# Kernel tuning notes

Hardware: AMD Instinct MI355X
Metric: run time of the kernel (lower is better)

The kernel has to match this reference:

```python
import jax, jax.numpy as jnp
import numpy as np

N, E, G = 10000, 160000, 64      # nodes, edges, graphs
IN, H, L = 128, 128, 14          # in_channels, hidden, num GENConv layers
EPS_LN = 1e-5                    # torch LayerNorm eps
EPS_MSG = 1e-7                   # GENConv message eps


def layer_norm(x, g, b):
    mu = jnp.mean(x, axis=-1, keepdims=True)
    v = jnp.var(x, axis=-1, keepdims=True)
    return (x - mu) * jax.lax.rsqrt(v + EPS_LN) * g + b


def gen_conv(h, src, dst, t, sc, W1, b1, mg, mb, W2, b2):
    # message: relu(x_j) + eps  (no edge_attr)
    msg = jax.nn.relu(h[src]) + EPS_MSG                      # [E, H]
    # softmax aggregation over edges sharing a destination, per feature
    z = msg * t
    mx = jax.ops.segment_max(z, dst, num_segments=N)         # [N, H]
    mx = jnp.where(jnp.isfinite(mx), mx, 0.0)
    e = jnp.exp(z - mx[dst])
    ssum = jax.ops.segment_sum(e, dst, num_segments=N)
    alpha = e / (ssum[dst] + 1e-16)
    agg = jax.ops.segment_sum(msg * alpha, dst, num_segments=N)  # [N, H]
    # MessageNorm: normalize(agg) * ||h|| * scale
    agg = agg / jnp.maximum(jnp.linalg.norm(agg, axis=-1, keepdims=True), 1e-12)
    agg = agg * jnp.linalg.norm(h, axis=-1, keepdims=True) * sc
    out = h + agg
    # MLP [H, 2H, H] with LayerNorm + ReLU between (dropout off in eval)
    z1 = layer_norm(out @ W1 + b1, mg, mb)
    return jax.nn.relu(z1) @ W2 + b2


def setup_inputs() -> dict:
    key = jax.random.key(0)
    ks = jax.random.split(key, 8)
    s = 0.05
    x = jax.random.normal(ks[0], (N, IN), jnp.float32)
    edge_index = jax.random.randint(ks[1], (2, E), 0, N, dtype=jnp.int64)
    batch = jnp.sort(jax.random.randint(ks[2], (N,), 0, G, dtype=jnp.int64))
    enc_W = jax.random.normal(ks[3], (IN, H), jnp.float32) * s
    enc_b = jnp.zeros((H,), jnp.float32)
    ln_g = jnp.ones((L, H), jnp.float32)
    ln_b = jnp.zeros((L, H), jnp.float32)
    t = jnp.ones((L,), jnp.float32)         # learnable softmax temperature
    scale = jnp.ones((L,), jnp.float32)     # learnable MsgNorm scale
    W1 = jax.random.normal(ks[4], (L, H, 2 * H), jnp.float32) * s
    b1 = jnp.zeros((L, 2 * H), jnp.float32)
    mg = jnp.ones((L, 2 * H), jnp.float32)
    mb = jnp.zeros((L, 2 * H), jnp.float32)
    W2 = jax.random.normal(ks[5], (L, 2 * H, H), jnp.float32) * s
    b2 = jnp.zeros((L, H), jnp.float32)
    fn_g = jnp.ones((H,), jnp.float32)
    fn_b = jnp.zeros((H,), jnp.float32)
    return dict(x=x, edge_index=edge_index, batch=batch, enc_W=enc_W, enc_b=enc_b,
                ln_g=ln_g, ln_b=ln_b, t=t, scale=scale, W1=W1, b1=b1, mg=mg, mb=mb,
                W2=W2, b2=b2, fn_g=fn_g, fn_b=fn_b)


def reference(x, edge_index, batch, enc_W, enc_b, ln_g, ln_b, t, scale,
              W1, b1, mg, mb, W2, b2, fn_g, fn_b):
    src, dst = edge_index[0], edge_index[1]
    h = x @ enc_W + enc_b
    for i in range(L):  # DeepGCNLayer 'res+': x + conv(act(norm(x)))
        r = jax.nn.leaky_relu(layer_norm(h, ln_g[i], ln_b[i]), 0.01)
        h = h + gen_conv(r, src, dst, t[i], scale[i],
                         W1[i], b1[i], mg[i], mb[i], W2[i], b2[i])
    h = jax.nn.leaky_relu(layer_norm(h, fn_g, fn_b), 0.01)
    # global_mean_pool (fin_map is unused in the original forward)
    cnt = jax.ops.segment_sum(jnp.ones((N,), h.dtype), batch, num_segments=G)
    gf = jax.ops.segment_sum(h, batch, num_segments=G) / jnp.maximum(cnt, 1.0)[:, None]
    return gf
```

## Files before the change

### kernel.cpp

```cpp
#include <hip/hip_runtime.h>
#include <cstdint>
#include <cstddef>


#define BT 512

typedef __attribute__((ext_vector_type(8))) short bf16x8;
typedef __attribute__((ext_vector_type(4))) float f32x4;

__device__ inline float bf2f(ushort u) {
    union { uint i; float f; } v;
    v.i = (uint)u << 16;
    return v.f;
}
__device__ inline ushort f2bf(float f) {
    union { float f; uint i; } v;
    v.f = f;
    return (ushort)((v.i + 0x7fffu + ((v.i >> 16) & 1u)) >> 16);
}
__device__ inline uint f2bf2(float a, float b) {
    return (uint)f2bf(a) | ((uint)f2bf(b) << 16);
}
__device__ inline float fast_exp2(float x) {
    return __builtin_amdgcn_exp2f(x);
}

__device__ inline float wave_sum_f(float v) {
#pragma unroll
    for (int off = 32; off > 0; off >>= 1) v += __shfl_xor(v, off, 64);
    return v;
}

__global__ void setup_kernel(const float* __restrict__ x, ushort* __restrict__ xb,
                             const int* __restrict__ dst, int* __restrict__ deg,
                             const int* __restrict__ batch, int* __restrict__ gstart,
                             int total, int N, int E, int G) {
    int idx = blockIdx.x * blockDim.x + threadIdx.x;
    if (idx >= total) return;
    xb[idx] = f2bf(x[idx]);
    if (idx < E) atomicAdd(&deg[dst[idx]], 1);
    if (idx < N) {
        int bb = batch[idx];
        if (idx == 0)
            for (int g = 0; g <= bb; g++) gstart[g] = 0;
        else {
            int pb = batch[idx - 1];
            for (int g = pb + 1; g <= bb; g++) gstart[g] = idx;
        }
        if (idx == N - 1)
            for (int g = bb + 1; g <= G; g++) gstart[g] = N;
    }
}

__global__ __launch_bounds__(1024) void scan_kernel(const int* __restrict__ deg,
                                                    int* __restrict__ offs,
                                                    int* __restrict__ cursor, int N) {
    __shared__ int part[1024];
    int tid = threadIdx.x;
    int CH = (N + 1023) / 1024;
    int base = tid * CH;
    int s = 0;
    for (int i = 0; i < CH; i++) {
        int idx = base + i;
        if (idx < N) s += deg[idx];
    }
    part[tid] = s;
    __syncthreads();
    for (int off = 1; off < 1024; off <<= 1) {
        int v = (tid >= off) ? part[tid - off] : 0;
        __syncthreads();
        part[tid] += v;
        __syncthreads();
    }
    int run = (tid == 0) ? 0 : part[tid - 1];
    for (int i = 0; i < CH; i++) {
        int idx = base + i;
        if (idx < N) {
            offs[idx] = run;
            cursor[idx] = run;
            run += deg[idx];
        }
    }
    if (tid == 1023) offs[N] = part[1023];
}

__global__ void scatter_kernel(const int* __restrict__ src, const int* __restrict__ dst,
                               int* __restrict__ cursor, int* __restrict__ esrc, int E) {
    int e = blockIdx.x * blockDim.x + threadIdx.x;
    if (e < E) {
        int d = dst[e];
        int pos = atomicAdd(&cursor[d], 1);
        esrc[pos] = src[e];
    }
}

__global__ __launch_bounds__(256) void prep_kernel(const float* __restrict__ W1,
                                                   const float* __restrict__ W2,
                                                   const float* __restrict__ encW,
                                                   ushort* __restrict__ W1t,
                                                   ushort* __restrict__ W2t,
                                                   ushort* __restrict__ encWt, int L) {
    __shared__ float tile[32][33];
    int z = blockIdx.z;
    const float* in;
    ushort* out;
    int R, C;
    if (z < L) {
        in = W1 + (size_t)z * 32768; out = W1t + (size_t)z * 32768; R = 128; C = 256;
    } else if (z < 2 * L) {
        int i = z - L;
        in = W2 + (size_t)i * 32768; out = W2t + (size_t)i * 32768; R = 256; C = 128;
    } else {
        in = encW; out = encWt; R = 128; C = 128;
    }
    int r0 = blockIdx.y * 32, c0 = blockIdx.x * 32;
    if (r0 >= R || c0 >= C) return;
    int tx = threadIdx.x & 31, ty = threadIdx.x >> 5;
    for (int i = ty; i < 32; i += 8) tile[i][tx] = in[(size_t)(r0 + i) * C + c0 + tx];
    __syncthreads();
    for (int i = ty; i < 32; i += 8)
        out[(size_t)(c0 + i) * R + r0 + tx] = f2bf(tile[tx][i]);
}

__device__ __forceinline__ void agg_stage_v18(const ushort* __restrict__ rin,
                                              const int* __restrict__ offs,
                                              const int* __restrict__ esrc,
                                              const float* __restrict__ rnbuf,
                                              float tv2, float sv,
                                              int row0, int w, int l,
                                              uint (*AsU)[68]) {
    const uint2* rin2 = (const uint2*)rin;
    int nd0 = row0 + 2 * w;
    int half = l >> 5, li = l & 31;
    int a0 = offs[nd0], a1 = offs[nd0 + 1], a2 = offs[nd0 + 2];
    int eb[2] = {a0, a1};
    int dg[2] = {a1 - a0, a2 - a1};

    uint2 ru0 = rin2[(size_t)nd0 * 32 + li];
    uint2 ru1 = rin2[(size_t)(nd0 + 1) * 32 + li];
    float rn0 = rnbuf[nd0], rn1 = rnbuf[nd0 + 1];

    float s[2][4] = {}, W[2][4] = {};
    int mxdeg = max(dg[0], dg[1]);

#pragma unroll 1
    for (int base = 0; base < mxdeg; base += 64) {
        int rem0 = min(dg[0] - base, 64);
        int rem1 = min(dg[1] - base, 64);
        int idx0 = (rem0 > 0 && l < rem0) ? esrc[eb[0] + base + l] : 0;
        int idx1 = (rem1 > 0 && l < rem1) ? esrc[eb[1] + base + l] : 0;
        int it = (max(rem0, rem1) + 7) >> 3;
#pragma unroll 1
        for (int i = 0; i < it; i++) {
            int j0 = i * 8 + half;
            uint2 rv[2][4];
            bool vl[2][4];
#pragma unroll
            for (int c = 0; c < 4; c++) {
                int j = j0 + 2 * c;
                vl[0][c] = j < rem0;
                vl[1][c] = j < rem1;
                int sn0 = __shfl(idx0, j, 64);
                int sn1 = __shfl(idx1, j, 64);
                if (vl[0][c]) rv[0][c] = rin2[(size_t)sn0 * 32 + li];
                if (vl[1][c]) rv[1][c] = rin2[(size_t)sn1 * 32 + li];
            }
#pragma unroll
            for (int k = 0; k < 2; k++)
#pragma unroll
                for (int c = 0; c < 4; c++) {
                    if (vl[k][c]) {
                        float f0 = bf2f((ushort)(rv[k][c].x & 0xffff));
                        float f1 = bf2f((ushort)(rv[k][c].x >> 16));
                        float f2 = bf2f((ushort)(rv[k][c].y & 0xffff));
                        float f3 = bf2f((ushort)(rv[k][c].y >> 16));
                        float g0 = fmaxf(f0, 0.f) + 1e-7f;
                        float g1 = fmaxf(f1, 0.f) + 1e-7f;
                        float g2 = fmaxf(f2, 0.f) + 1e-7f;
                        float g3 = fmaxf(f3, 0.f) + 1e-7f;
                        float p0 = fast_exp2(g0 * tv2);
                        float p1 = fast_exp2(g1 * tv2);
                        float p2 = fast_exp2(g2 * tv2);
                        float p3 = fast_exp2(g3 * tv2);
                        s[k][0] += p0; W[k][0] += g0 * p0;
                        s[k][1] += p1; W[k][1] += g1 * p1;
                        s[k][2] += p2; W[k][2] += g2 * p2;
                        s[k][3] += p3; W[k][3] += g3 * p3;
                    }
                }
        }
    }

#pragma unroll
    for (int k = 0; k < 2; k++) {
#pragma unroll
        for (int f = 0; f < 4; f++) {
            s[k][f] += __shfl_xor(s[k][f], 32, 64);
            W[k][f] += __shfl_xor(W[k][f], 32, 64);
        }
        float agg[4], nsq = 0.f;
#pragma unroll
        for (int f = 0; f < 4; f++) {
            agg[f] = W[k][f] / (s[k][f] + 1e-16f);
            nsq += agg[f] * agg[f];
        }
#pragma unroll
        for (int off = 1; off < 32; off <<= 1) nsq += __shfl_xor(nsq, off, 64);
        float rnv = (k == 0) ? rn0 : rn1;
        uint2 ru = (k == 0) ? ru0 : ru1;
        float fac = rnv * sv / fmaxf(sqrtf(nsq), 1e-12f);
        if (half == 0) {
            uint2 o;
            o.x = f2bf2(bf2f((ushort)(ru.x & 0xffff)) + agg[0] * fac,
                        bf2f((ushort)(ru.x >> 16)) + agg[1] * fac);
            o.y = f2bf2(bf2f((ushort)(ru.y & 0xffff)) + agg[2] * fac,
                        bf2f((ushort)(ru.y >> 16)) + agg[3] * fac);
            *(uint2*)&AsU[2 * w + k][2 * li] = o;
        }
    }
}

__device__ __forceinline__ void gemm1_stage8(const ushort (*As)[136],
                                             const ushort* __restrict__ Bt,
                                             const float* __restrict__ bias,
                                             const float* __restrict__ mg,
                                             const float* __restrict__ mb,
                                             ushort (*z1s)[264],
                                             int w, int q, int ln,
                                             float (*pS)[16], float (*pQ)[16]) {
    f32x4 acc[2];
    acc[0] = (f32x4){0.f, 0.f, 0.f, 0.f};
    acc[1] = (f32x4){0.f, 0.f, 0.f, 0.f};
#pragma unroll
    for (int ks = 0; ks < 128; ks += 32) {
        bf16x8 a = *(const bf16x8*)&As[ln][ks + q * 8];
#pragma unroll
        for (int ct = 0; ct < 2; ct++) {
            bf16x8 bv = *(const bf16x8*)(Bt + (size_t)(w * 32 + ct * 16 + ln) * 128 + ks + q * 8);
            acc[ct] = __builtin_amdgcn_mfma_f32_16x16x32_bf16(a, bv, acc[ct], 0, 0, 0);
        }
    }
    float s1[4] = {0, 0, 0, 0}, s2[4] = {0, 0, 0, 0};
#pragma unroll
    for (int ct = 0; ct < 2; ct++)
#pragma unroll
        for (int r = 0; r < 4; r++) {
            float v = acc[ct][r] + bias[w * 32 + ct * 16 + ln];
            acc[ct][r] = v;
            s1[r] += v;
            s2[r] += v * v;
        }
#pragma unroll
    for (int off = 1; off < 16; off <<= 1)
#pragma unroll
        for (int r = 0; r < 4; r++) {
            s1[r] += __shfl_xor(s1[r], off, 64);
            s2[r] += __shfl_xor(s2[r], off, 64);
        }
    if (ln == 0)
#pragma unroll
        for (int r = 0; r < 4; r++) {
            pS[w][q * 4 + r] = s1[r];
            pQ[w][q * 4 + r] = s2[r];
        }
    __syncthreads();
#pragma unroll
    for (int r = 0; r < 4; r++) {
        int row = q * 4 + r;
        float S = 0.f, Q = 0.f;
#pragma unroll
        for (int ww = 0; ww < 8; ww++) {
            S += pS[ww][row];
            Q += pQ[ww][row];
        }
        float mu = S * (1.f / 256.f);
        float var = Q * (1.f / 256.f) - mu * mu;
        float rs = rsqrtf(var + 1e-5f);
#pragma unroll
        for (int ct = 0; ct < 2; ct++) {
            int col = w * 32 + ct * 16 + ln;
            float y = (acc[ct][r] - mu) * rs * mg[col] + mb[col];
            z1s[row][col] = f2bf(fmaxf(y, 0.f));
        }
    }
    __syncthreads();
}

template <int KD, bool RESID>
__device__ __forceinline__ void out_stage8(const ushort* __restrict__ Abase, int astr,
                                           const ushort* __restrict__ Bt,
                                           const float* __restrict__ bias,
                                           const float* __restrict__ lg,
                                           const float* __restrict__ lb,
                                           float* __restrict__ hbuf,
                                           ushort* __restrict__ rout,
                                           float* __restrict__ rnbuf,
                                           int row0, int w, int q, int ln,
                                           float (*pS)[16], float (*pQ)[16]) {
    f32x4 acc = (f32x4){0.f, 0.f, 0.f, 0.f};
    int col = w * 16 + ln;
#pragma unroll
    for (int ks = 0; ks < KD; ks += 32) {
        bf16x8 a = *(const bf16x8*)(Abase + ln * astr + ks + q * 8);
        bf16x8 bv = *(const bf16x8*)(Bt + (size_t)col * KD + ks + q * 8);
        acc = __builtin_amdgcn_mfma_f32_16x16x32_bf16(a, bv, acc, 0, 0, 0);
    }
    float s1[4], s2[4];
#pragma unroll
    for (int r = 0; r < 4; r++) {
        int row = q * 4 + r;
        float v = acc[r] + bias[col];
        if (RESID) v += hbuf[(size_t)(row0 + row) * 128 + col];
        hbuf[(size_t)(row0 + row) * 128 + col] = v;
        acc[r] = v;
        s1[r] = v;
        s2[r] = v * v;
    }
#pragma unroll
    for (int off = 1; off < 16; off <<= 1)
#pragma unroll
        for (int r = 0; r < 4; r++) {
            s1[r] += __shfl_xor(s1[r], off, 64);
            s2[r] += __shfl_xor(s2[r], off, 64);
        }
    if (ln == 0)
#pragma unroll
        for (int r = 0; r < 4; r++) {
            pS[w][q * 4 + r] = s1[r];
            pQ[w][q * 4 + r] = s2[r];
        }
    __syncthreads();
    float yv[4];
    float t2[4];
#pragma unroll
    for (int r = 0; r < 4; r++) {
        int row = q * 4 + r;
        float S = 0.f, Q = 0.f;
#pragma unroll
        for (int ww = 0; ww < 8; ww++) {
            S += pS[ww][row];
            Q += pQ[ww][row];
        }
        float mu = S * (1.f / 128.f);
        float var = Q * (1.f / 128.f) - mu * mu;
        float rs = rsqrtf(var + 1e-5f);
        float y = (acc[r] - mu) * rs * lg[col] + lb[col];
        y = y > 0.f ? y : 0.01f * y;
        yv[r] = y;
        t2[r] = y * y;
    }
#pragma unroll
    for (int off = 1; off < 16; off <<= 1)
#pragma unroll
        for (int r = 0; r < 4; r++) t2[r] += __shfl_xor(t2[r], off, 64);
    __syncthreads();
    if (ln == 0)
#pragma unroll
        for (int r = 0; r < 4; r++) pS[w][q * 4 + r] = t2[r];
    __syncthreads();
#pragma unroll
    for (int r = 0; r < 4; r++) {
        int row = q * 4 + r;
        float T = 0.f;
#pragma unroll
        for (int ww = 0; ww < 8; ww++) T += pS[ww][row];
        if (w == 0 && ln == 0) rnbuf[row0 + row] = sqrtf(T);
        rout[(size_t)(row0 + row) * 128 + col] = f2bf(yv[r]);
    }
}

__global__ __launch_bounds__(BT) void enc_kernel(const ushort* __restrict__ xb,
                                                 const ushort* __restrict__ encWt,
                                                 const float* __restrict__ encB,
                                                 const float* __restrict__ lg,
                                                 const float* __restrict__ lb,
                                                 float* __restrict__ h,
                                                 ushort* __restrict__ rbuf,
                                                 float* __restrict__ rn, int N) {
    __shared__ __align__(16) ushort As[16][136];
    __shared__ float pS[8][16], pQ[8][16];
    uint(*AsU)[68] = (uint(*)[68])As;
    int tid = threadIdx.x, w = tid >> 6, l = tid & 63;
    int q = l >> 4, ln = l & 15;
    int row0 = blockIdx.x * 16;
    for (int idx = tid; idx < 16 * 64; idx += BT) {
        int row = idx >> 6, cl = idx & 63;
        AsU[row][cl] = ((const uint*)xb)[(size_t)(row0 + row) * 64 + cl];
    }
    __syncthreads();
    out_stage8<128, false>(&As[0][0], 136, encWt, encB, lg, lb, h, rbuf, rn,
                           row0, w, q, ln, pS, pQ);
}

__global__ __launch_bounds__(BT) void layer_kernel(const ushort* __restrict__ rin,
                                                   ushort* __restrict__ rout,
                                                   const int* __restrict__ offs,
                                                   const int* __restrict__ esrc,
                                                   float* __restrict__ rn,
                                                   float* __restrict__ h,
                                                   const ushort* __restrict__ W1t,
                                                   const ushort* __restrict__ W2t,
                                                   const float* __restrict__ b1,
                                                   const float* __restrict__ mg,
                                                   const float* __restrict__ mb,
                                                   const float* __restrict__ b2,
                                                   const float* __restrict__ ng,
                                                   const float* __restrict__ nb,
                                                   const float* __restrict__ tptr,
                                                   const float* __restrict__ scptr,
                                                   int N) {
    __shared__ __align__(16) ushort As[16][136];
    __shared__ __align__(16) ushort z1s[16][264];
    __shared__ float pS[8][16], pQ[8][16];
    uint(*AsU)[68] = (uint(*)[68])As;
    int tid = threadIdx.x, w = tid >> 6, l = tid & 63;
    int q = l >> 4, ln = l & 15;
    int row0 = blockIdx.x * 16;
    float tv2 = (*tptr) * 1.4426950408889634f;
    float sv = *scptr;
    agg_stage_v18(rin, offs, esrc, rn, tv2, sv, row0, w, l, AsU);
    __syncthreads();
    gemm1_stage8(As, W1t, b1, mg, mb, z1s, w, q, ln, pS, pQ);
    out_stage8<256, true>(&z1s[0][0], 264, W2t, b2, ng, nb, h, rout, rn,
                          row0, w, q, ln, pS, pQ);
}

__global__ __launch_bounds__(256) void pool_kernel(const ushort* __restrict__ rf,
                                                   const int* __restrict__ gstart,
                                                   float* __restrict__ out) {
    __shared__ float pb0[4][64], pb1[4][64];
    int g = blockIdx.x;
    int w = threadIdx.x >> 6, l = threadIdx.x & 63;
    int s = gstart[g], e = gstart[g + 1];
    float a0 = 0.f, a1 = 0.f;
    for (int n = s + w; n < e; n += 4) {
        uint rv = ((const uint*)rf)[(size_t)n * 64 + l];
        a0 += bf2f((ushort)(rv & 0xffff));
        a1 += bf2f((ushort)(rv >> 16));
    }
    pb0[w][l] = a0;
    pb1[w][l] = a1;
    __syncthreads();
    if (threadIdx.x < 64) {
        float t0 = pb0[0][l] + pb0[1][l] + pb0[2][l] + pb0[3][l];
        float t1 = pb1[0][l] + pb1[1][l] + pb1[2][l] + pb1[3][l];
        float inv = 1.f / fmaxf((float)(e - s), 1.f);
        out[g * 128 + 2 * l] = t0 * inv;
        out[g * 128 + 2 * l + 1] = t1 * inv;
    }
}

extern "C" void kernel_launch(void* const* d_in, const int* in_sizes, int n_in,
                              void* d_out, int out_size, void* d_ws, size_t ws_size,
                              hipStream_t stream) {
    const float* x     = (const float*)d_in[0];
    const int*   ei    = (const int*)d_in[1];
    const int*   batch = (const int*)d_in[2];
    const float* encW  = (const float*)d_in[3];
    const float* encB  = (const float*)d_in[4];
    const float* ln_g  = (const float*)d_in[5];
    const float* ln_b  = (const float*)d_in[6];
    const float* tArr  = (const float*)d_in[7];
    const float* scArr = (const float*)d_in[8];
    const float* W1    = (const float*)d_in[9];
    const float* b1    = (const float*)d_in[10];
    const float* mg    = (const float*)d_in[11];
    const float* mb    = (const float*)d_in[12];
    const float* W2    = (const float*)d_in[13];
    const float* b2    = (const float*)d_in[14];
    const float* fn_g  = (const float*)d_in[15];
    const float* fn_b  = (const float*)d_in[16];
    float* out = (float*)d_out;

    const int N = in_sizes[0] / 128;
    const int E = in_sizes[1] / 2;
    const int L = in_sizes[7];
    const int G = 64;

    const int* src = ei;
    const int* dst = ei + E;

    char* p = (char*)d_ws;
    auto alloc = [&](size_t bytes) -> void* {
        void* qp = (void*)p;
        p += (bytes + 255) & ~(size_t)255;
        return qp;
    };
    int*    deg    = (int*)alloc((size_t)N * 4);
    int*    offs   = (int*)alloc((size_t)(N + 1) * 4);
    int*    cursor = (int*)alloc((size_t)N * 4);
    int*    esrc   = (int*)alloc((size_t)E * 4);
    int*    gstart = (int*)alloc((size_t)(G + 1) * 4);
    float*  h      = (float*)alloc((size_t)N * 128 * 4);
    ushort* r0     = (ushort*)alloc((size_t)N * 128 * 2);
    ushort* r1     = (ushort*)alloc((size_t)N * 128 * 2);
    float*  rn     = (float*)alloc((size_t)N * 4);
    ushort* xb     = (ushort*)alloc((size_t)N * 128 * 2);
    ushort* W1t    = (ushort*)alloc((size_t)L * 32768 * 2);
    ushort* W2t    = (ushort*)alloc((size_t)L * 32768 * 2);
    ushort* encWt  = (ushort*)alloc((size_t)16384 * 2);

    (void)hipMemsetAsync(deg, 0, (size_t)N * 4, stream);

    setup_kernel<<<(N * 128 + 255) / 256, 256, 0, stream>>>(x, xb, dst, deg, batch,
                                                            gstart, N * 128, N, E, G);
    scan_kernel<<<1, 1024, 0, stream>>>(deg, offs, cursor, N);
    scatter_kernel<<<(E + 255) / 256, 256, 0, stream>>>(src, dst, cursor, esrc, E);
    prep_kernel<<<dim3(8, 8, 2 * L + 1), 256, 0, stream>>>(W1, W2, encW, W1t, W2t,
                                                           encWt, L);

    const int TILES = N / 16;

    enc_kernel<<<TILES, BT, 0, stream>>>(xb, encWt, encB, ln_g, ln_b, h, r0, rn, N);

    for (int i = 0; i < L; i++) {
        const ushort* rin = (i & 1) ? r1 : r0;
        ushort* rout = (i & 1) ? r0 : r1;
        const float* ng = (i < L - 1) ? (ln_g + (size_t)(i + 1) * 128) : fn_g;
        const float* nb = (i < L - 1) ? (ln_b + (size_t)(i + 1) * 128) : fn_b;
        layer_kernel<<<TILES, BT, 0, stream>>>(rin, rout, offs, esrc, rn, h,
                                               W1t + ((size_t)i << 15),
                                               W2t + ((size_t)i << 15),
                                               b1 + (size_t)i * 256,
                                               mg + (size_t)i * 256,
                                               mb + (size_t)i * 256,
                                               b2 + (size_t)i * 128,
                                               ng, nb, tArr + i, scArr + i, N);
    }

    const ushort* rf = ((L - 1) & 1) ? r0 : r1;
    pool_kernel<<<G, 256, 0, stream>>>(rf, gstart, out);
}
```

Baseline: 579.0 us.

## Sort nodes by in-degree so layer tiles group similar-degree nodes

```diff
diff --git a/kernel.cpp b/kernel.cpp
--- a/kernel.cpp
+++ b/kernel.cpp
@@ -23,12 +23,6 @@
 }
 __device__ inline float fast_exp2(float x) {
     return __builtin_amdgcn_exp2f(x);
-}
-
-__device__ inline float wave_sum_f(float v) {
-#pragma unroll
-    for (int off = 32; off > 0; off >>= 1) v += __shfl_xor(v, off, 64);
-    return v;
 }
 
 __global__ void setup_kernel(const float* __restrict__ x, ushort* __restrict__ xb,
@@ -91,6 +85,35 @@
         int d = dst[e];
         int pos = atomicAdd(&cursor[d], 1);
         esrc[pos] = src[e];
+    }
+}
+
+__global__ __launch_bounds__(1024) void sort_kernel(const int* __restrict__ offs,
+                                                    int* __restrict__ perm, int N) {
+    __shared__ int hist[256];
+    __shared__ int cur[256];
+    int tid = threadIdx.x;
+    if (tid < 256) hist[tid] = 0;
+    __syncthreads();
+    for (int n = tid; n < N; n += 1024) {
+        int d = offs[n + 1] - offs[n];
+        int key = 255 - min(d, 255);
+        atomicAdd(&hist[key], 1);
+    }
+    __syncthreads();
+    if (tid == 0) {
+        int run = 0;
+        for (int i = 0; i < 256; i++) {
+            cur[i] = run;
+            run += hist[i];
+        }
+    }
+    __syncthreads();
+    for (int n = tid; n < N; n += 1024) {
+        int d = offs[n + 1] - offs[n];
+        int key = 255 - min(d, 255);
+        int pos = atomicAdd(&cur[key], 1);
+        perm[pos] = n;
     }
 }
 
@@ -122,23 +145,22 @@
         out[(size_t)(c0 + i) * R + r0 + tx] = f2bf(tile[tx][i]);
 }
 
-__device__ __forceinline__ void agg_stage_v18(const ushort* __restrict__ rin,
+__device__ __forceinline__ void agg_stage_v19(const ushort* __restrict__ rin,
                                               const int* __restrict__ offs,
                                               const int* __restrict__ esrc,
                                               const float* __restrict__ rnbuf,
                                               float tv2, float sv,
-                                              int row0, int w, int l,
-                                              uint (*AsU)[68]) {
+                                              int nd0, int nd1,
+                                              int w, int l, uint (*AsU)[68]) {
     const uint2* rin2 = (const uint2*)rin;
-    int nd0 = row0 + 2 * w;
     int half = l >> 5, li = l & 31;
-    int a0 = offs[nd0], a1 = offs[nd0 + 1], a2 = offs[nd0 + 2];
-    int eb[2] = {a0, a1};
-    int dg[2] = {a1 - a0, a2 - a1};
+    int eb[2], dg[2];
+    eb[0] = offs[nd0]; dg[0] = offs[nd0 + 1] - eb[0];
+    eb[1] = offs[nd1]; dg[1] = offs[nd1 + 1] - eb[1];
 
     uint2 ru0 = rin2[(size_t)nd0 * 32 + li];
-    uint2 ru1 = rin2[(size_t)(nd0 + 1) * 32 + li];
-    float rn0 = rnbuf[nd0], rn1 = rnbuf[nd0 + 1];
+    uint2 ru1 = rin2[(size_t)nd1 * 32 + li];
+    float rn0 = rnbuf[nd0], rn1 = rnbuf[nd1];
 
     float s[2][4] = {}, W[2][4] = {};
     int mxdeg = max(dg[0], dg[1]);
@@ -295,7 +317,8 @@
                                            float* __restrict__ hbuf,
                                            ushort* __restrict__ rout,
                                            float* __restrict__ rnbuf,
-                                           int row0, int w, int q, int ln,
+                                           const int* rowmap,
+                                           int w, int q, int ln,
                                            float (*pS)[16], float (*pQ)[16]) {
     f32x4 acc = (f32x4){0.f, 0.f, 0.f, 0.f};
     int col = w * 16 + ln;
@@ -308,10 +331,10 @@
     float s1[4], s2[4];
 #pragma unroll
     for (int r = 0; r < 4; r++) {
-        int row = q * 4 + r;
+        int grow = rowmap[q * 4 + r];
         float v = acc[r] + bias[col];
-        if (RESID) v += hbuf[(size_t)(row0 + row) * 128 + col];
-        hbuf[(size_t)(row0 + row) * 128 + col] = v;
+        if (RESID) v += hbuf[(size_t)grow * 128 + col];
+        hbuf[(size_t)grow * 128 + col] = v;
         acc[r] = v;
         s1[r] = v;
         s2[r] = v * v;
@@ -360,12 +383,12 @@
     __syncthreads();
 #pragma unroll
     for (int r = 0; r < 4; r++) {
-        int row = q * 4 + r;
+        int grow = rowmap[q * 4 + r];
         float T = 0.f;
 #pragma unroll
-        for (int ww = 0; ww < 8; ww++) T += pS[ww][row];
-        if (w == 0 && ln == 0) rnbuf[row0 + row] = sqrtf(T);
-        rout[(size_t)(row0 + row) * 128 + col] = f2bf(yv[r]);
+        for (int ww = 0; ww < 8; ww++) T += pS[ww][q * 4 + r];
+        if (w == 0 && ln == 0) rnbuf[grow] = sqrtf(T);
+        rout[(size_t)grow * 128 + col] = f2bf(yv[r]);
     }
 }
 
@@ -379,23 +402,26 @@
                                                  float* __restrict__ rn, int N) {
     __shared__ __align__(16) ushort As[16][136];
     __shared__ float pS[8][16], pQ[8][16];
+    __shared__ int rowmap[16];
     uint(*AsU)[68] = (uint(*)[68])As;
     int tid = threadIdx.x, w = tid >> 6, l = tid & 63;
     int q = l >> 4, ln = l & 15;
     int row0 = blockIdx.x * 16;
+    if (tid < 16) rowmap[tid] = row0 + tid;
     for (int idx = tid; idx < 16 * 64; idx += BT) {
         int row = idx >> 6, cl = idx & 63;
         AsU[row][cl] = ((const uint*)xb)[(size_t)(row0 + row) * 64 + cl];
     }
     __syncthreads();
     out_stage8<128, false>(&As[0][0], 136, encWt, encB, lg, lb, h, rbuf, rn,
-                           row0, w, q, ln, pS, pQ);
+                           rowmap, w, q, ln, pS, pQ);
 }
 
 __global__ __launch_bounds__(BT) void layer_kernel(const ushort* __restrict__ rin,
                                                    ushort* __restrict__ rout,
                                                    const int* __restrict__ offs,
                                                    const int* __restrict__ esrc,
+                                                   const int* __restrict__ perm,
                                                    float* __restrict__ rn,
                                                    float* __restrict__ h,
                                                    const ushort* __restrict__ W1t,
@@ -412,17 +438,21 @@
     __shared__ __align__(16) ushort As[16][136];
     __shared__ __align__(16) ushort z1s[16][264];
     __shared__ float pS[8][16], pQ[8][16];
+    __shared__ int rowmap[16];
     uint(*AsU)[68] = (uint(*)[68])As;
     int tid = threadIdx.x, w = tid >> 6, l = tid & 63;
     int q = l >> 4, ln = l & 15;
     int row0 = blockIdx.x * 16;
+    if (tid < 16) rowmap[tid] = perm[row0 + tid];
+    __syncthreads();
     float tv2 = (*tptr) * 1.4426950408889634f;
     float sv = *scptr;
-    agg_stage_v18(rin, offs, esrc, rn, tv2, sv, row0, w, l, AsU);
+    agg_stage_v19(rin, offs, esrc, rn, tv2, sv,
+                  rowmap[2 * w], rowmap[2 * w + 1], w, l, AsU);
     __syncthreads();
     gemm1_stage8(As, W1t, b1, mg, mb, z1s, w, q, ln, pS, pQ);
     out_stage8<256, true>(&z1s[0][0], 264, W2t, b2, ng, nb, h, rout, rn,
-                          row0, w, q, ln, pS, pQ);
+                          rowmap, w, q, ln, pS, pQ);
 }
 
 __global__ __launch_bounds__(256) void pool_kernel(const ushort* __restrict__ rf,
@@ -491,6 +521,7 @@
     int*    cursor = (int*)alloc((size_t)N * 4);
     int*    esrc   = (int*)alloc((size_t)E * 4);
     int*    gstart = (int*)alloc((size_t)(G + 1) * 4);
+    int*    perm   = (int*)alloc((size_t)N * 4);
     float*  h      = (float*)alloc((size_t)N * 128 * 4);
     ushort* r0     = (ushort*)alloc((size_t)N * 128 * 2);
     ushort* r1     = (ushort*)alloc((size_t)N * 128 * 2);
@@ -506,6 +537,7 @@
                                                             gstart, N * 128, N, E, G);
     scan_kernel<<<1, 1024, 0, stream>>>(deg, offs, cursor, N);
     scatter_kernel<<<(E + 255) / 256, 256, 0, stream>>>(src, dst, cursor, esrc, E);
+    sort_kernel<<<1, 1024, 0, stream>>>(offs, perm, N);
     prep_kernel<<<dim3(8, 8, 2 * L + 1), 256, 0, stream>>>(W1, W2, encW, W1t, W2t,
                                                            encWt, L);
 
@@ -518,7 +550,7 @@
         ushort* rout = (i & 1) ? r0 : r1;
         const float* ng = (i < L - 1) ? (ln_g + (size_t)(i + 1) * 128) : fn_g;
         const float* nb = (i < L - 1) ? (ln_b + (size_t)(i + 1) * 128) : fn_b;
-        layer_kernel<<<TILES, BT, 0, stream>>>(rin, rout, offs, esrc, rn, h,
+        layer_kernel<<<TILES, BT, 0, stream>>>(rin, rout, offs, esrc, perm, rn, h,
                                                W1t + ((size_t)i << 15),
                                                W2t + ((size_t)i << 15),
                                                b1 + (size_t)i * 256,
```

Result: no change. 570.8 us (-1.4%).
